# Performance work log

Hardware: AMD Instinct MI355X
Metric: run time of the kernel (lower is better)

Reference implementation:

```python
import jax, jax.numpy as jnp
import numpy as np

N_NODES = 50000
N_EDGES = 800000
D = 128  # in_dim == hidden_dim


def setup_inputs() -> dict:
    key = jax.random.key(0)
    k1, k2, k3, k4 = jax.random.split(key, 4)
    x = jax.random.normal(k1, (N_NODES, D), dtype=jnp.float32)
    edge_index = jax.random.randint(k2, (2, N_EDGES), 0, N_NODES, dtype=jnp.int64)
    # Glorot-ish scale for square weights
    scale = 1.0 / np.sqrt(D)
    W1 = jax.random.normal(k3, (D, D), dtype=jnp.float32) * scale
    W2 = jax.random.normal(k4, (D, D), dtype=jnp.float32) * scale
    b1 = jnp.zeros((D,), dtype=jnp.float32)
    b2 = jnp.zeros((D,), dtype=jnp.float32)
    return {"x": x, "edge_index": edge_index, "W1": W1, "b1": b1, "W2": W2, "b2": b2}


def _gcn_layer(x, W, b, src, dst, norm, n):
    # PyG GCNConv: h = x @ W, then symmetric-normalized scatter-add, then + bias
    h = x @ W                                   # [N, D] dense GEMM
    msg = h[src] * norm[:, None]                # [E', D] gather + scale
    out = jax.ops.segment_sum(msg, dst, num_segments=n)  # scatter-add
    return out + b


def reference(x, edge_index, W1, b1, W2, b2):
    n = x.shape[0]
    # add self-loops (GCNConv default add_self_loops=True)
    loops = jnp.arange(n, dtype=edge_index.dtype)
    src = jnp.concatenate([edge_index[0], loops])
    dst = jnp.concatenate([edge_index[1], loops])
    # symmetric normalization: deg^{-1/2}[src] * deg^{-1/2}[dst]
    deg = jax.ops.segment_sum(jnp.ones_like(src, dtype=x.dtype), dst, num_segments=n)
    dinv = jax.lax.rsqrt(jnp.maximum(deg, 1.0))  # deg >= 1 due to self-loops
    norm = dinv[src] * dinv[dst]
    # layer 1: conv -> relu (dropout is identity in eval mode)
    h = jax.nn.relu(_gcn_layer(x, W1, b1, src, dst, norm, n))
    # layer 2 (cut='c2'): conv -> relu
    h = jax.nn.relu(_gcn_layer(h, W2, b2, src, dst, norm, n))
    return h
```

## Files before the change

kernel.cpp:

```cpp
#include <hip/hip_runtime.h>

#define NN 50000
#define NE 800000
#define DD 128
#define NSTRIP 3125
#define NB 196
#define CHUNK 4096
#define MAXB 6144

#define OF_LCNT  0
#define OF_LOFS  50176
#define OF_DINV  100352
#define OF_OFFS2 150528
#define OF_TMP2  250624
#define OF_CSRU  1053440
#define OF_H1    1655552
#define OF_H2    4855552
#define OF_W1H   8055552
#define OF_W1L   8063744
#define OF_W2H   8071936
#define OF_W2L   8080128

typedef __attribute__((ext_vector_type(8))) short bf8_t;
typedef __attribute__((ext_vector_type(8))) unsigned short us8;
typedef __attribute__((ext_vector_type(4))) float f32x4;

static __device__ __forceinline__ unsigned short f2bf(float f) {
    unsigned int u = __float_as_uint(f);
    unsigned int r = (u + 0x7fffu + ((u >> 16) & 1u)) >> 16;
    return (unsigned short)r;
}
static __device__ __forceinline__ float bf2f(unsigned short h) {
    return __uint_as_float(((unsigned int)h) << 16);
}

__global__ void k_wconv(const float* __restrict__ W1, const float* __restrict__ W2,
                        ushort* __restrict__ w1h, ushort* __restrict__ w1l,
                        ushort* __restrict__ w2h, ushort* __restrict__ w2l) {
    int gg = blockIdx.x * 256 + threadIdx.x;
    const float* W = (gg < 2048) ? W1 : W2;
    ushort* wh = (gg < 2048) ? w1h : w2h;
    ushort* wl = (gg < 2048) ? w1l : w2l;
    int g = gg & 2047;
    int ntile = g >> 8;
    int kk = (g >> 6) & 3;
    int lane = g & 63;
    int k0 = kk * 32 + ((lane >> 4) * 8);
    int col = ntile * 16 + (lane & 15);
#pragma unroll
    for (int j = 0; j < 8; ++j) {
        float w = W[(k0 + j) * DD + col];
        unsigned short h = f2bf(w);
        wh[(size_t)g * 8 + j] = h;
        wl[(size_t)g * 8 + j] = f2bf(w - bf2f(h));
    }
}

__global__ __launch_bounds__(256) void k_prep(
        const int* __restrict__ src, const int* __restrict__ dst,
        int* __restrict__ lcnt_g, int* __restrict__ lofs_g,
        unsigned int* __restrict__ tmp2,
        const float* __restrict__ X,
        const ushort* __restrict__ wh, const ushort* __restrict__ wl,
        ushort* __restrict__ H1) {
    __shared__ int lcnt[256];
    __shared__ int lsc[256];
    __shared__ int lcur[256];
    int tid = threadIdx.x;
    if (blockIdx.x < 196) {
        int blk = blockIdx.x;
        lcnt[tid] = 0;
        __syncthreads();
        int e0 = blk * CHUNK;
        int e1 = e0 + CHUNK; if (e1 > NE) e1 = NE;
        for (int e = e0 + tid; e < e1; e += 256)
            atomicAdd(&lcnt[dst[e] >> 8], 1);
        __syncthreads();
        int v = lcnt[tid];
        lsc[tid] = v;
        __syncthreads();
        for (int o = 1; o < 256; o <<= 1) {
            int t = (tid >= o) ? lsc[tid - o] : 0;
            __syncthreads();
            lsc[tid] += t;
            __syncthreads();
        }
        int excl = lsc[tid] - v;
        lcnt_g[tid * 196 + blk] = v;
        lofs_g[tid * 196 + blk] = excl;
        lcur[tid] = excl;
        __syncthreads();
        for (int e = e0 + tid; e < e1; e += 256) {
            int d = dst[e], s = src[e];
            int b = d >> 8;
            int r = atomicAdd(&lcur[b], 1);
            tmp2[blk * CHUNK + r] = ((unsigned int)s << 8) | (unsigned int)(d & 255);
        }
        return;
    }
    int wave = tid >> 6;
    int lane = tid & 63;
    int strip = (blockIdx.x - 196) * 4 + wave;
    if (strip >= NSTRIP) return;
    int rb = strip << 4;
    int m = lane & 15;
    int quad = lane >> 4;
    const float* ar = X + (size_t)(rb + m) * DD;
    f32x4 acc[8];
#pragma unroll
    for (int t = 0; t < 8; ++t) acc[t] = (f32x4){0.f, 0.f, 0.f, 0.f};
#pragma unroll
    for (int kk = 0; kk < 4; ++kk) {
        float4 xa = *(const float4*)(ar + kk * 32 + quad * 8);
        float4 xb = *(const float4*)(ar + kk * 32 + quad * 8 + 4);
        float xs[8] = {xa.x, xa.y, xa.z, xa.w, xb.x, xb.y, xb.z, xb.w};
        bf8_t ah, al;
#pragma unroll
        for (int j = 0; j < 8; ++j) {
            unsigned short hh = f2bf(xs[j]);
            ah[j] = (short)hh;
            al[j] = (short)f2bf(xs[j] - bf2f(hh));
        }
#pragma unroll
        for (int t = 0; t < 8; ++t) {
            size_t bo = ((size_t)(t * 4 + kk) * 64 + lane) * 8;
            bf8_t bh = *(const bf8_t*)(wh + bo);
            bf8_t bl = *(const bf8_t*)(wl + bo);
            acc[t] = __builtin_amdgcn_mfma_f32_16x16x32_bf16(ah, bh, acc[t], 0, 0, 0);
            acc[t] = __builtin_amdgcn_mfma_f32_16x16x32_bf16(ah, bl, acc[t], 0, 0, 0);
            acc[t] = __builtin_amdgcn_mfma_f32_16x16x32_bf16(al, bh, acc[t], 0, 0, 0);
        }
    }
#pragma unroll
    for (int t = 0; t < 8; ++t) {
#pragma unroll
        for (int r = 0; r < 4; ++r)
            H1[(size_t)(rb + quad * 4 + r) * DD + t * 16 + m] = f2bf(acc[t][r]);
    }
}

__global__ __launch_bounds__(256) void k_sort(const int* __restrict__ lcnt_g,
                                              const int* __restrict__ lofs_g,
                                              const unsigned int* __restrict__ tmp2,
                                              ushort* __restrict__ csru,
                                              int2* __restrict__ offs2,
                                              float* __restrict__ dinv) {
    __shared__ unsigned int ent[MAXB];
    __shared__ int c[256];
    __shared__ int p[256];
    __shared__ int o[256];
    __shared__ int cnt[256];
    __shared__ int boff[256];
    __shared__ int cur[256];
    int b = blockIdx.x, tid = threadIdx.x;
    int cv = (tid < 196) ? lcnt_g[b * 196 + tid] : 0;
    o[tid] = (tid < 196) ? lofs_g[b * 196 + tid] : 0;
    c[tid] = cv;
    p[tid] = cv;
    cnt[tid] = 0;
    __syncthreads();
    for (int s = 1; s < 256; s <<= 1) {
        int t = (tid >= s) ? p[tid - s] : 0;
        __syncthreads();
        p[tid] += t;
        __syncthreads();
    }
    int nb = p[255];
    for (int i = tid; i < nb; i += 256) {
        int lo = 0, hi = 255;
#pragma unroll
        for (int it = 0; it < 8; ++it) {
            int mid = (lo + hi) >> 1;
            if (p[mid] > i) hi = mid; else lo = mid + 1;
        }
        int blk = lo;
        int j = i - (p[blk] - c[blk]);
        unsigned int e = tmp2[blk * CHUNK + o[blk] + j];
        ent[i] = e;
        atomicAdd(&cnt[e & 255], 1);
    }
    __syncthreads();
    int v = cnt[tid];
    boff[tid] = v;
    __syncthreads();
    for (int s = 1; s < 256; s <<= 1) {
        int t = (tid >= s) ? boff[tid - s] : 0;
        __syncthreads();
        boff[tid] += t;
        __syncthreads();
    }
    int excl = boff[tid] - v;
    int base = b * MAXB;
    int node = b * 256 + tid;
    if (node < NN) {
        offs2[node] = make_int2(base + excl, base + excl + v);
        dinv[node] = rsqrtf((float)(v + 1));
    }
    cur[tid] = excl;
    __syncthreads();
    for (int i = tid; i < nb; i += 256) {
        unsigned int e = ent[i];
        int bin = e & 255;
        int r = atomicAdd(&cur[bin], 1);
        csru[base + r] = (ushort)(e >> 8);
    }
}

__global__ __launch_bounds__(512) void k_aggmm(const ushort* __restrict__ h1,
                                               const float* __restrict__ dinv,
                                               const int2* __restrict__ offs2,
                                               const ushort* __restrict__ csru,
                                               const float* __restrict__ b1,
                                               const ushort* __restrict__ w2h,
                                               const ushort* __restrict__ w2l,
                                               ushort* __restrict__ h2) {
    __shared__ float xs[16][136];
    int wave = threadIdx.x >> 6;
    int lane = threadIdx.x & 63;
    int rb = blockIdx.x * 16;
    int q = lane >> 4;
    int l = lane & 15;
    const float* bp = b1 + 8 * l;
    for (int nn = 0; nn < 2; ++nn) {
        int node = rb + wave * 2 + nn;
        float a0[8] = {0.f, 0.f, 0.f, 0.f, 0.f, 0.f, 0.f, 0.f};
        float a1[8] = {0.f, 0.f, 0.f, 0.f, 0.f, 0.f, 0.f, 0.f};
        float a2[8] = {0.f, 0.f, 0.f, 0.f, 0.f, 0.f, 0.f, 0.f};
        float a3[8] = {0.f, 0.f, 0.f, 0.f, 0.f, 0.f, 0.f, 0.f};
        int2 oe = offs2[node];
        int e  = oe.x + q;
        int e1 = oe.y;
        for (; e + 12 < e1; e += 16) {
            int s0 = csru[e];
            int s1 = csru[e + 4];
            int s2 = csru[e + 8];
            int s3 = csru[e + 12];
            float w0 = dinv[s0], w1 = dinv[s1], w2 = dinv[s2], w3 = dinv[s3];
            us8 v0 = *(const us8*)(h1 + (size_t)s0 * DD + 8 * l);
            us8 v1 = *(const us8*)(h1 + (size_t)s1 * DD + 8 * l);
            us8 v2 = *(const us8*)(h1 + (size_t)s2 * DD + 8 * l);
            us8 v3 = *(const us8*)(h1 + (size_t)s3 * DD + 8 * l);
#pragma unroll
            for (int j = 0; j < 8; ++j) {
                a0[j] += w0 * bf2f(v0[j]);
                a1[j] += w1 * bf2f(v1[j]);
                a2[j] += w2 * bf2f(v2[j]);
                a3[j] += w3 * bf2f(v3[j]);
            }
        }
        for (; e < e1; e += 4) {
            int s0 = csru[e];
            float w0 = dinv[s0];
            us8 v0 = *(const us8*)(h1 + (size_t)s0 * DD + 8 * l);
#pragma unroll
            for (int j = 0; j < 8; ++j) a0[j] += w0 * bf2f(v0[j]);
        }
        float dnode = dinv[node];
        if (q == 0) {
            us8 v = *(const us8*)(h1 + (size_t)node * DD + 8 * l);
#pragma unroll
            for (int j = 0; j < 8; ++j) a0[j] += dnode * bf2f(v[j]);
        }
#pragma unroll
        for (int j = 0; j < 8; ++j) {
            a0[j] += a1[j] + a2[j] + a3[j];
            a0[j] += __shfl_xor(a0[j], 16, 64);
            a0[j] += __shfl_xor(a0[j], 32, 64);
        }
        if (q == 0) {
            float* xr = &xs[wave * 2 + nn][8 * l];
#pragma unroll
            for (int j = 0; j < 8; ++j)
                xr[j] = fmaxf(dnode * a0[j] + bp[j], 0.f);
        }
    }
    __syncthreads();
    int m = lane & 15;
    int quad = lane >> 4;
    int t = wave;
    f32x4 acc = (f32x4){0.f, 0.f, 0.f, 0.f};
#pragma unroll
    for (int kk = 0; kk < 4; ++kk) {
        const float* xr = &xs[m][kk * 32 + quad * 8];
        float4 xa = *(const float4*)xr;
        float4 xb = *(const float4*)(xr + 4);
        float xv[8] = {xa.x, xa.y, xa.z, xa.w, xb.x, xb.y, xb.z, xb.w};
        bf8_t ah, al;
#pragma unroll
        for (int j = 0; j < 8; ++j) {
            unsigned short hh = f2bf(xv[j]);
            ah[j] = (short)hh;
            al[j] = (short)f2bf(xv[j] - bf2f(hh));
        }
        size_t bo = ((size_t)(t * 4 + kk) * 64 + lane) * 8;
        bf8_t bh = *(const bf8_t*)(w2h + bo);
        bf8_t bl = *(const bf8_t*)(w2l + bo);
        acc = __builtin_amdgcn_mfma_f32_16x16x32_bf16(ah, bh, acc, 0, 0, 0);
        acc = __builtin_amdgcn_mfma_f32_16x16x32_bf16(ah, bl, acc, 0, 0, 0);
        acc = __builtin_amdgcn_mfma_f32_16x16x32_bf16(al, bh, acc, 0, 0, 0);
    }
#pragma unroll
    for (int r = 0; r < 4; ++r)
        h2[(size_t)(rb + quad * 4 + r) * DD + t * 16 + m] = f2bf(acc[r]);
}

__global__ void k_agg(const ushort* __restrict__ h, const float* __restrict__ dinv,
                      const int2* __restrict__ offs2, const ushort* __restrict__ csru,
                      const float* __restrict__ bias, float* __restrict__ outf) {
    int wave = threadIdx.x >> 6;
    int lane = threadIdx.x & 63;
    int node = blockIdx.x * 4 + wave;
    int q = lane >> 4;
    int l = lane & 15;
    float a0[8] = {0.f, 0.f, 0.f, 0.f, 0.f, 0.f, 0.f, 0.f};
    float a1[8] = {0.f, 0.f, 0.f, 0.f, 0.f, 0.f, 0.f, 0.f};
    float a2[8] = {0.f, 0.f, 0.f, 0.f, 0.f, 0.f, 0.f, 0.f};
    float a3[8] = {0.f, 0.f, 0.f, 0.f, 0.f, 0.f, 0.f, 0.f};
    int2 oe = offs2[node];
    int e  = oe.x + q;
    int e1 = oe.y;
    for (; e + 12 < e1; e += 16) {
        int s0 = csru[e];
        int s1 = csru[e + 4];
        int s2 = csru[e + 8];
        int s3 = csru[e + 12];
        float w0 = dinv[s0], w1 = dinv[s1], w2 = dinv[s2], w3 = dinv[s3];
        us8 v0 = *(const us8*)(h + (size_t)s0 * DD + 8 * l);
        us8 v1 = *(const us8*)(h + (size_t)s1 * DD + 8 * l);
        us8 v2 = *(const us8*)(h + (size_t)s2 * DD + 8 * l);
        us8 v3 = *(const us8*)(h + (size_t)s3 * DD + 8 * l);
#pragma unroll
        for (int j = 0; j < 8; ++j) {
            a0[j] += w0 * bf2f(v0[j]);
            a1[j] += w1 * bf2f(v1[j]);
            a2[j] += w2 * bf2f(v2[j]);
            a3[j] += w3 * bf2f(v3[j]);
        }
    }
    for (; e < e1; e += 4) {
        int s0 = csru[e];
        float w0 = dinv[s0];
        us8 v0 = *(const us8*)(h + (size_t)s0 * DD + 8 * l);
#pragma unroll
        for (int j = 0; j < 8; ++j) a0[j] += w0 * bf2f(v0[j]);
    }
    float dnode = dinv[node];
    if (q == 0) {
        us8 v = *(const us8*)(h + (size_t)node * DD + 8 * l);
#pragma unroll
        for (int j = 0; j < 8; ++j) a0[j] += dnode * bf2f(v[j]);
    }
#pragma unroll
    for (int j = 0; j < 8; ++j) {
        a0[j] += a1[j] + a2[j] + a3[j];
        a0[j] += __shfl_xor(a0[j], 16, 64);
        a0[j] += __shfl_xor(a0[j], 32, 64);
    }
    if (q == 0) {
        float* op = outf + (size_t)node * DD + 8 * l;
        const float* bp = bias + 8 * l;
        float4 o0, o1;
        o0.x = fmaxf(dnode * a0[0] + bp[0], 0.f);
        o0.y = fmaxf(dnode * a0[1] + bp[1], 0.f);
        o0.z = fmaxf(dnode * a0[2] + bp[2], 0.f);
        o0.w = fmaxf(dnode * a0[3] + bp[3], 0.f);
        o1.x = fmaxf(dnode * a0[4] + bp[4], 0.f);
        o1.y = fmaxf(dnode * a0[5] + bp[5], 0.f);
        o1.z = fmaxf(dnode * a0[6] + bp[6], 0.f);
        o1.w = fmaxf(dnode * a0[7] + bp[7], 0.f);
        *(float4*)op = o0;
        *(float4*)(op + 4) = o1;
    }
}

extern "C" void kernel_launch(void* const* d_in, const int* in_sizes, int n_in,
                              void* d_out, int out_size, void* d_ws, size_t ws_size,
                              hipStream_t stream) {
    const float* x  = (const float*)d_in[0];
    const int*   ei = (const int*)d_in[1];
    const float* W1 = (const float*)d_in[2];
    const float* b1 = (const float*)d_in[3];
    const float* W2 = (const float*)d_in[4];
    const float* b2 = (const float*)d_in[5];
    float* out = (float*)d_out;

    const int* src = ei;
    const int* dst = ei + NE;

    int*          wsi  = (int*)d_ws;
    float*        wsf  = (float*)d_ws;
    ushort*       wsu  = (ushort*)d_ws;
    unsigned int* wsuw = (unsigned int*)d_ws;
    int*    lcnt_g = wsi + OF_LCNT;
    int*    lofs_g = wsi + OF_LOFS;
    float*  dinv   = wsf + OF_DINV;
    int2*   offs2  = (int2*)(wsi + OF_OFFS2);
    unsigned int* tmp2 = wsuw + OF_TMP2;
    ushort* csru   = wsu + (size_t)OF_CSRU * 2;
    ushort* h1     = wsu + (size_t)OF_H1 * 2;
    ushort* h2     = wsu + (size_t)OF_H2 * 2;
    ushort* w1h    = wsu + (size_t)OF_W1H * 2;
    ushort* w1l    = wsu + (size_t)OF_W1L * 2;
    ushort* w2h    = wsu + (size_t)OF_W2H * 2;
    ushort* w2l    = wsu + (size_t)OF_W2L * 2;

    hipLaunchKernelGGL(k_wconv, dim3(16), dim3(256), 0, stream,
                       W1, W2, w1h, w1l, w2h, w2l);
    hipLaunchKernelGGL(k_prep, dim3(196 + (NSTRIP + 3) / 4), dim3(256), 0, stream,
                       src, dst, lcnt_g, lofs_g, tmp2, x, w1h, w1l, h1);
    hipLaunchKernelGGL(k_sort, dim3(NB), dim3(256), 0, stream,
                       lcnt_g, lofs_g, tmp2, csru, offs2, dinv);
    hipLaunchKernelGGL(k_aggmm, dim3(NSTRIP), dim3(512), 0, stream,
                       h1, dinv, offs2, csru, b1, w2h, w2l, h2);
    hipLaunchKernelGGL(k_agg, dim3(NN / 4), dim3(256), 0, stream,
                       h2, dinv, offs2, csru, b2, out);
}
```

Baseline: 210.2 us.

## Precompute per-edge fp16 normalization weights packed with source index in CSR

Counts global in-degrees with atomics in the prep kernel so the sort kernel can compute each edge's full symmetric norm, dinv[src]*dinv[dst]. That norm is packed as fp16 next to the 16-bit source index in a 32-bit CSR entry. Both aggregation kernels then drop the dependent dinv[src] gather and the final dnode scale, and process 8 edges per lane per iteration with clamped, masked loads in a single accumulator. This adds per-edge global atomics on deg, doubles the CSR storage, and rounds edge weights to fp16.

```diff
diff --git a/kernel.cpp b/kernel.cpp
--- a/kernel.cpp
+++ b/kernel.cpp
@@ -1,4 +1,5 @@
 #include <hip/hip_runtime.h>
+#include <hip/hip_fp16.h>
 
 #define NN 50000
 #define NE 800000
@@ -11,15 +12,16 @@
 #define OF_LCNT  0
 #define OF_LOFS  50176
 #define OF_DINV  100352
-#define OF_OFFS2 150528
-#define OF_TMP2  250624
-#define OF_CSRU  1053440
-#define OF_H1    1655552
-#define OF_H2    4855552
-#define OF_W1H   8055552
-#define OF_W1L   8063744
-#define OF_W2H   8071936
-#define OF_W2L   8080128
+#define OF_DEG   150352
+#define OF_OFFS2 200352
+#define OF_TMP2  300352
+#define OF_CSRW  1103168
+#define OF_H1    2307392
+#define OF_H2    5507392
+#define OF_W1H   8707392
+#define OF_W1L   8715584
+#define OF_W2H   8723776
+#define OF_W2L   8731968
 
 typedef __attribute__((ext_vector_type(8))) short bf8_t;
 typedef __attribute__((ext_vector_type(8))) unsigned short us8;
@@ -36,8 +38,10 @@
 
 __global__ void k_wconv(const float* __restrict__ W1, const float* __restrict__ W2,
                         ushort* __restrict__ w1h, ushort* __restrict__ w1l,
-                        ushort* __restrict__ w2h, ushort* __restrict__ w2l) {
+                        ushort* __restrict__ w2h, ushort* __restrict__ w2l,
+                        int* __restrict__ deg) {
     int gg = blockIdx.x * 256 + threadIdx.x;
+    for (int i = gg; i < NN; i += 4096) deg[i] = 0;
     const float* W = (gg < 2048) ? W1 : W2;
     ushort* wh = (gg < 2048) ? w1h : w2h;
     ushort* wl = (gg < 2048) ? w1l : w2l;
@@ -59,7 +63,7 @@
 __global__ __launch_bounds__(256) void k_prep(
         const int* __restrict__ src, const int* __restrict__ dst,
         int* __restrict__ lcnt_g, int* __restrict__ lofs_g,
-        unsigned int* __restrict__ tmp2,
+        unsigned int* __restrict__ tmp2, int* __restrict__ deg,
         const float* __restrict__ X,
         const ushort* __restrict__ wh, const ushort* __restrict__ wl,
         ushort* __restrict__ H1) {
@@ -73,8 +77,11 @@
         __syncthreads();
         int e0 = blk * CHUNK;
         int e1 = e0 + CHUNK; if (e1 > NE) e1 = NE;
-        for (int e = e0 + tid; e < e1; e += 256)
-            atomicAdd(&lcnt[dst[e] >> 8], 1);
+        for (int e = e0 + tid; e < e1; e += 256) {
+            int d = dst[e];
+            atomicAdd(&lcnt[d >> 8], 1);
+            atomicAdd(&deg[d], 1);
+        }
         __syncthreads();
         int v = lcnt[tid];
         lsc[tid] = v;
@@ -142,7 +149,8 @@
 __global__ __launch_bounds__(256) void k_sort(const int* __restrict__ lcnt_g,
                                               const int* __restrict__ lofs_g,
                                               const unsigned int* __restrict__ tmp2,
-                                              ushort* __restrict__ csru,
+                                              const int* __restrict__ deg,
+                                              unsigned int* __restrict__ csrw,
                                               int2* __restrict__ offs2,
                                               float* __restrict__ dinv) {
     __shared__ unsigned int ent[MAXB];
@@ -152,6 +160,7 @@
     __shared__ int cnt[256];
     __shared__ int boff[256];
     __shared__ int cur[256];
+    __shared__ float sdv[256];
     int b = blockIdx.x, tid = threadIdx.x;
     int cv = (tid < 196) ? lcnt_g[b * 196 + tid] : 0;
     o[tid] = (tid < 196) ? lofs_g[b * 196 + tid] : 0;
@@ -192,24 +201,29 @@
     int excl = boff[tid] - v;
     int base = b * MAXB;
     int node = b * 256 + tid;
+    float dv = rsqrtf((float)(v + 1));
+    sdv[tid] = dv;
     if (node < NN) {
         offs2[node] = make_int2(base + excl, base + excl + v);
-        dinv[node] = rsqrtf((float)(v + 1));
+        dinv[node] = dv;
     }
     cur[tid] = excl;
     __syncthreads();
     for (int i = tid; i < nb; i += 256) {
         unsigned int e = ent[i];
         int bin = e & 255;
+        int s = (int)(e >> 8);
         int r = atomicAdd(&cur[bin], 1);
-        csru[base + r] = (ushort)(e >> 8);
+        float w = rsqrtf((float)(deg[s] + 1)) * sdv[bin];
+        csrw[base + r] = ((unsigned int)s << 16) |
+                         (unsigned int)__half_as_ushort(__float2half(w));
     }
 }
 
 __global__ __launch_bounds__(512) void k_aggmm(const ushort* __restrict__ h1,
                                                const float* __restrict__ dinv,
                                                const int2* __restrict__ offs2,
-                                               const ushort* __restrict__ csru,
+                                               const unsigned int* __restrict__ csrw,
                                                const float* __restrict__ b1,
                                                const ushort* __restrict__ w2h,
                                                const ushort* __restrict__ w2l,
@@ -223,55 +237,49 @@
     const float* bp = b1 + 8 * l;
     for (int nn = 0; nn < 2; ++nn) {
         int node = rb + wave * 2 + nn;
-        float a0[8] = {0.f, 0.f, 0.f, 0.f, 0.f, 0.f, 0.f, 0.f};
-        float a1[8] = {0.f, 0.f, 0.f, 0.f, 0.f, 0.f, 0.f, 0.f};
-        float a2[8] = {0.f, 0.f, 0.f, 0.f, 0.f, 0.f, 0.f, 0.f};
-        float a3[8] = {0.f, 0.f, 0.f, 0.f, 0.f, 0.f, 0.f, 0.f};
         int2 oe = offs2[node];
-        int e  = oe.x + q;
         int e1 = oe.y;
-        for (; e + 12 < e1; e += 16) {
-            int s0 = csru[e];
-            int s1 = csru[e + 4];
-            int s2 = csru[e + 8];
-            int s3 = csru[e + 12];
-            float w0 = dinv[s0], w1 = dinv[s1], w2 = dinv[s2], w3 = dinv[s3];
-            us8 v0 = *(const us8*)(h1 + (size_t)s0 * DD + 8 * l);
-            us8 v1 = *(const us8*)(h1 + (size_t)s1 * DD + 8 * l);
-            us8 v2 = *(const us8*)(h1 + (size_t)s2 * DD + 8 * l);
-            us8 v3 = *(const us8*)(h1 + (size_t)s3 * DD + 8 * l);
+        float a[8] = {0.f, 0.f, 0.f, 0.f, 0.f, 0.f, 0.f, 0.f};
+        for (int eb = oe.x; eb < e1; eb += 32) {
+            int s[8]; float w[8];
 #pragma unroll
             for (int j = 0; j < 8; ++j) {
-                a0[j] += w0 * bf2f(v0[j]);
-                a1[j] += w1 * bf2f(v1[j]);
-                a2[j] += w2 * bf2f(v2[j]);
-                a3[j] += w3 * bf2f(v3[j]);
+                int e = eb + q + 4 * j;
+                int er = (e < e1) ? e : (e1 - 1);
+                er = (er < 0) ? 0 : er;
+                unsigned int rw = csrw[er];
+                s[j] = (int)(rw >> 16);
+                w[j] = (e < e1)
+                     ? __half2float(__ushort_as_half((unsigned short)(rw & 0xffffu)))
+                     : 0.f;
             }
-        }
-        for (; e < e1; e += 4) {
-            int s0 = csru[e];
-            float w0 = dinv[s0];
-            us8 v0 = *(const us8*)(h1 + (size_t)s0 * DD + 8 * l);
-#pragma unroll
-            for (int j = 0; j < 8; ++j) a0[j] += w0 * bf2f(v0[j]);
+            us8 v[8];
+#pragma unroll
+            for (int j = 0; j < 8; ++j)
+                v[j] = *(const us8*)(h1 + ((size_t)s[j] << 7) + 8 * l);
+#pragma unroll
+            for (int j = 0; j < 8; ++j) {
+#pragma unroll
+                for (int d = 0; d < 8; ++d) a[d] += w[j] * bf2f(v[j][d]);
+            }
         }
         float dnode = dinv[node];
         if (q == 0) {
-            us8 v = *(const us8*)(h1 + (size_t)node * DD + 8 * l);
-#pragma unroll
-            for (int j = 0; j < 8; ++j) a0[j] += dnode * bf2f(v[j]);
+            us8 v = *(const us8*)(h1 + ((size_t)node << 7) + 8 * l);
+            float ws = dnode * dnode;
+#pragma unroll
+            for (int j = 0; j < 8; ++j) a[j] += ws * bf2f(v[j]);
         }
 #pragma unroll
         for (int j = 0; j < 8; ++j) {
-            a0[j] += a1[j] + a2[j] + a3[j];
-            a0[j] += __shfl_xor(a0[j], 16, 64);
-            a0[j] += __shfl_xor(a0[j], 32, 64);
+            a[j] += __shfl_xor(a[j], 16, 64);
+            a[j] += __shfl_xor(a[j], 32, 64);
         }
         if (q == 0) {
             float* xr = &xs[wave * 2 + nn][8 * l];
 #pragma unroll
             for (int j = 0; j < 8; ++j)
-                xr[j] = fmaxf(dnode * a0[j] + bp[j], 0.f);
+                xr[j] = fmaxf(a[j] + bp[j], 0.f);
         }
     }
     __syncthreads();
@@ -304,70 +312,67 @@
         h2[(size_t)(rb + quad * 4 + r) * DD + t * 16 + m] = f2bf(acc[r]);
 }
 
-__global__ void k_agg(const ushort* __restrict__ h, const float* __restrict__ dinv,
-                      const int2* __restrict__ offs2, const ushort* __restrict__ csru,
-                      const float* __restrict__ bias, float* __restrict__ outf) {
+__global__ __launch_bounds__(256) void k_agg(const ushort* __restrict__ h,
+                                             const float* __restrict__ dinv,
+                                             const int2* __restrict__ offs2,
+                                             const unsigned int* __restrict__ csrw,
+                                             const float* __restrict__ bias,
+                                             float* __restrict__ outf) {
     int wave = threadIdx.x >> 6;
     int lane = threadIdx.x & 63;
     int node = blockIdx.x * 4 + wave;
     int q = lane >> 4;
     int l = lane & 15;
-    float a0[8] = {0.f, 0.f, 0.f, 0.f, 0.f, 0.f, 0.f, 0.f};
-    float a1[8] = {0.f, 0.f, 0.f, 0.f, 0.f, 0.f, 0.f, 0.f};
-    float a2[8] = {0.f, 0.f, 0.f, 0.f, 0.f, 0.f, 0.f, 0.f};
-    float a3[8] = {0.f, 0.f, 0.f, 0.f, 0.f, 0.f, 0.f, 0.f};
     int2 oe = offs2[node];
-    int e  = oe.x + q;
     int e1 = oe.y;
-    for (; e + 12 < e1; e += 16) {
-        int s0 = csru[e];
-        int s1 = csru[e + 4];
-        int s2 = csru[e + 8];
-        int s3 = csru[e + 12];
-        float w0 = dinv[s0], w1 = dinv[s1], w2 = dinv[s2], w3 = dinv[s3];
-        us8 v0 = *(const us8*)(h + (size_t)s0 * DD + 8 * l);
-        us8 v1 = *(const us8*)(h + (size_t)s1 * DD + 8 * l);
-        us8 v2 = *(const us8*)(h + (size_t)s2 * DD + 8 * l);
-        us8 v3 = *(const us8*)(h + (size_t)s3 * DD + 8 * l);
+    float a[8] = {0.f, 0.f, 0.f, 0.f, 0.f, 0.f, 0.f, 0.f};
+    for (int eb = oe.x; eb < e1; eb += 32) {
+        int s[8]; float w[8];
 #pragma unroll
         for (int j = 0; j < 8; ++j) {
-            a0[j] += w0 * bf2f(v0[j]);
-            a1[j] += w1 * bf2f(v1[j]);
-            a2[j] += w2 * bf2f(v2[j]);
-            a3[j] += w3 * bf2f(v3[j]);
-        }
-    }
-    for (; e < e1; e += 4) {
-        int s0 = csru[e];
-        float w0 = dinv[s0];
-        us8 v0 = *(const us8*)(h + (size_t)s0 * DD + 8 * l);
-#pragma unroll
-        for (int j = 0; j < 8; ++j) a0[j] += w0 * bf2f(v0[j]);
+            int e = eb + q + 4 * j;
+            int er = (e < e1) ? e : (e1 - 1);
+            er = (er < 0) ? 0 : er;
+            unsigned int rw = csrw[er];
+            s[j] = (int)(rw >> 16);
+            w[j] = (e < e1)
+                 ? __half2float(__ushort_as_half((unsigned short)(rw & 0xffffu)))
+                 : 0.f;
+        }
+        us8 v[8];
+#pragma unroll
+        for (int j = 0; j < 8; ++j)
+            v[j] = *(const us8*)(h + ((size_t)s[j] << 7) + 8 * l);
+#pragma unroll
+        for (int j = 0; j < 8; ++j) {
+#pragma unroll
+            for (int d = 0; d < 8; ++d) a[d] += w[j] * bf2f(v[j][d]);
+        }
     }
     float dnode = dinv[node];
     if (q == 0) {
-        us8 v = *(const us8*)(h + (size_t)node * DD + 8 * l);
-#pragma unroll
-        for (int j = 0; j < 8; ++j) a0[j] += dnode * bf2f(v[j]);
+        us8 v = *(const us8*)(h + ((size_t)node << 7) + 8 * l);
+        float ws = dnode * dnode;
+#pragma unroll
+        for (int j = 0; j < 8; ++j) a[j] += ws * bf2f(v[j]);
     }
 #pragma unroll
     for (int j = 0; j < 8; ++j) {
-        a0[j] += a1[j] + a2[j] + a3[j];
-        a0[j] += __shfl_xor(a0[j], 16, 64);
-        a0[j] += __shfl_xor(a0[j], 32, 64);
+        a[j] += __shfl_xor(a[j], 16, 64);
+        a[j] += __shfl_xor(a[j], 32, 64);
     }
     if (q == 0) {
         float* op = outf + (size_t)node * DD + 8 * l;
         const float* bp = bias + 8 * l;
         float4 o0, o1;
-        o0.x = fmaxf(dnode * a0[0] + bp[0], 0.f);
-        o0.y = fmaxf(dnode * a0[1] + bp[1], 0.f);
-        o0.z = fmaxf(dnode * a0[2] + bp[2], 0.f);
-        o0.w = fmaxf(dnode * a0[3] + bp[3], 0.f);
-        o1.x = fmaxf(dnode * a0[4] + bp[4], 0.f);
-        o1.y = fmaxf(dnode * a0[5] + bp[5], 0.f);
-        o1.z = fmaxf(dnode * a0[6] + bp[6], 0.f);
-        o1.w = fmaxf(dnode * a0[7] + bp[7], 0.f);
+        o0.x = fmaxf(a[0] + bp[0], 0.f);
+        o0.y = fmaxf(a[1] + bp[1], 0.f);
+        o0.z = fmaxf(a[2] + bp[2], 0.f);
+        o0.w = fmaxf(a[3] + bp[3], 0.f);
+        o1.x = fmaxf(a[4] + bp[4], 0.f);
+        o1.y = fmaxf(a[5] + bp[5], 0.f);
+        o1.z = fmaxf(a[6] + bp[6], 0.f);
+        o1.w = fmaxf(a[7] + bp[7], 0.f);
         *(float4*)op = o0;
         *(float4*)(op + 4) = o1;
     }
@@ -394,9 +399,10 @@
     int*    lcnt_g = wsi + OF_LCNT;
     int*    lofs_g = wsi + OF_LOFS;
     float*  dinv   = wsf + OF_DINV;
+    int*    deg    = wsi + OF_DEG;
     int2*   offs2  = (int2*)(wsi + OF_OFFS2);
     unsigned int* tmp2 = wsuw + OF_TMP2;
-    ushort* csru   = wsu + (size_t)OF_CSRU * 2;
+    unsigned int* csrw = wsuw + OF_CSRW;
     ushort* h1     = wsu + (size_t)OF_H1 * 2;
     ushort* h2     = wsu + (size_t)OF_H2 * 2;
     ushort* w1h    = wsu + (size_t)OF_W1H * 2;
@@ -405,13 +411,13 @@
     ushort* w2l    = wsu + (size_t)OF_W2L * 2;
 
     hipLaunchKernelGGL(k_wconv, dim3(16), dim3(256), 0, stream,
-                       W1, W2, w1h, w1l, w2h, w2l);
+                       W1, W2, w1h, w1l, w2h, w2l, deg);
     hipLaunchKernelGGL(k_prep, dim3(196 + (NSTRIP + 3) / 4), dim3(256), 0, stream,
-                       src, dst, lcnt_g, lofs_g, tmp2, x, w1h, w1l, h1);
+                       src, dst, lcnt_g, lofs_g, tmp2, deg, x, w1h, w1l, h1);
     hipLaunchKernelGGL(k_sort, dim3(NB), dim3(256), 0, stream,
-                       lcnt_g, lofs_g, tmp2, csru, offs2, dinv);
+                       lcnt_g, lofs_g, tmp2, deg, csrw, offs2, dinv);
     hipLaunchKernelGGL(k_aggmm, dim3(NSTRIP), dim3(512), 0, stream,
-                       h1, dinv, offs2, csru, b1, w2h, w2l, h2);
+                       h1, dinv, offs2, csrw, b1, w2h, w2l, h2);
     hipLaunchKernelGGL(k_agg, dim3(NN / 4), dim3(256), 0, stream,
-                       h2, dinv, offs2, csru, b2, out);
-}
+                       h2, dinv, offs2, csrw, b2, out);
+}
```

New measurement: 226.7 us. +7.8%, slower.
